# Kernel tuning notes

Hardware: AMD Instinct MI355X
Metric: run time of the kernel (lower is better)

Reference implementation:

```python
import jax, jax.numpy as jnp
import numpy as np

B, H, S, D = 4, 16, 2048, 128
NEG = -1000000000.0


def setup_inputs() -> dict:
    key = jax.random.key(0)
    kq, kk, kv, km = jax.random.split(key, 4)
    Q = jax.random.normal(kq, (B, H, S, D), dtype=jnp.float32)
    K = jax.random.normal(kk, (B, H, S, D), dtype=jnp.float32)
    V = jax.random.normal(kv, (B, H, S, D), dtype=jnp.float32)
    mask = jax.random.randint(km, (B, 1, S, S), 0, 2, dtype=jnp.int32)
    return {"Q": Q, "K": K, "V": V, "mask": mask}


def reference(Q, K, V, mask):
    # NOTE: original module computes d_k but never scales -> no 1/sqrt(d_k).
    scores = jnp.einsum("bhqd,bhkd->bhqk", Q, K)  # [B,H,S,S]
    scores = jnp.where(mask == 0, NEG, scores)
    attn = jax.nn.softmax(scores, axis=-1)
    out = jnp.einsum("bhqk,bhkd->bhqd", attn, V)  # [B,H,S,D]
    return out
```

## Files before the change

kernel.cpp:

```cpp
#include <hip/hip_runtime.h>
#include <hip/hip_bf16.h>

#define B_ 4
#define H_ 16
#define S_ 2048
#define D_ 128
#define NEGV -1000000000.0f
#define LOG2E 1.44269504f
#define THR 9.0f

typedef _Float16 f16;
typedef __attribute__((ext_vector_type(8))) _Float16 f16x8;
typedef __attribute__((ext_vector_type(4))) _Float16 f16x4v;
typedef __attribute__((ext_vector_type(2))) __fp16 fp16x2_b;
typedef __attribute__((ext_vector_type(4))) float f32x4;

__device__ inline unsigned int pack2h(float lo, float hi){
  union { f16 h[2]; unsigned int u; } cv;
  cv.h[0] = (f16)lo; cv.h[1] = (f16)hi;
  return cv.u;
}
__device__ inline unsigned short f2h16(float x){
  union { f16 h; unsigned short u; } cv; cv.h = (f16)x; return cv.u;
}
__device__ inline unsigned int pkrtz(float a, float b){
  union { fp16x2_b h; unsigned int u; } cv;
  cv.h = __builtin_amdgcn_cvt_pkrtz(a, b);
  return cv.u;
}
__device__ inline void async16(void* l, const void* g){
  __builtin_amdgcn_global_load_lds(
      (const __attribute__((address_space(1))) unsigned int*)g,
      (__attribute__((address_space(3))) unsigned int*)l, 16, 0, 0);
}

constexpr size_t MBW     = (size_t)B_*S_*(S_/32);
constexpr size_t KBYTES  = (size_t)B_*H_*S_*D_*2;
constexpr size_t WS_MID  = MBW*4 + 2*KBYTES;

__global__ __launch_bounds__(256)
void prepass(const float* __restrict__ K, const float* __restrict__ V,
             const int* __restrict__ mask, unsigned int* __restrict__ mbits,
             char* __restrict__ wsK, char* __restrict__ wsV)
{
  __shared__ char Vim[16384];
  int bid = blockIdx.x, tid = threadIdx.x;
  size_t base = (size_t)bid * (64*128);
  const float* kp = K + base;
  char* ok = wsK + (size_t)bid*16384;
  #pragma unroll
  for (int j = 0; j < 8; ++j){
    int f = tid + j*256; int kr = f>>5, c = f&31;
    float4 v = *(const float4*)(kp + kr*128 + c*4);
    unsigned int lo = pack2h(v.x, v.y), hi = pack2h(v.z, v.w);
    int off = (kr*256 + c*8) ^ ((kr&7)<<4);
    *(uint2*)(ok + off) = make_uint2(lo, hi);
  }
  const float* vp = V + base;
  #pragma unroll
  for (int j = 0; j < 8; ++j){
    int f = tid + j*256; int k = f>>5, c = f&31;
    float4 v = *(const float4*)(vp + k*128 + c*4);
    float e[4] = {v.x, v.y, v.z, v.w};
    #pragma unroll
    for (int u = 0; u < 4; ++u){
      int d = c*4 + u;
      *(unsigned short*)(Vim + d*128 + ((2*k) ^ ((d&7)<<4))) = f2h16(e[u]);
    }
  }
  __syncthreads();
  char* ov = wsV + (size_t)bid*16384;
  #pragma unroll
  for (int j = 0; j < 4; ++j)
    *(uint4*)(ov + tid*16 + j*4096) = *(const uint4*)(Vim + tid*16 + j*4096);
  {
    size_t wdx = (size_t)bid*256 + tid;
    const int* p = mask + wdx*32;
    unsigned int o = 0;
    #pragma unroll
    for (int i = 0; i < 32; i += 4){
      int4 m4 = *(const int4*)(p + i);
      o |= (m4.x ? 1u<<i : 0u) | (m4.y ? 1u<<(i+1) : 0u)
         | (m4.z ? 1u<<(i+2) : 0u) | (m4.w ? 1u<<(i+3) : 0u);
    }
    mbits[wdx] = o;
  }
}

__global__ __launch_bounds__(256, 2)
void attn_fast(const float* __restrict__ Q,
               const unsigned long long* __restrict__ mbits,
               const char* __restrict__ wsK, const char* __restrict__ wsV,
               float* __restrict__ out)
{
  __shared__ char KB[2][16384];
  __shared__ char VB[2][16384];
  __shared__ char PL[8192];

  int bid = blockIdx.x;
  int wg = (bid & 7) * 128 + (bid >> 3);
  int bh = wg >> 4, qb = wg & 15;
  int b  = bh >> 4;
  int tid = threadIdx.x;
  int w = tid >> 6, lane = tid & 63;
  int g = lane >> 4, r = lane & 15;
  int sw = (r & 7) << 4;
  size_t base = (size_t)bh * (S_*D_);
  int qg0 = qb*128 + w*32 + r;
  int qg1 = qg0 + 16;

  f16x8 qf[2][4];
  #pragma unroll
  for (int u = 0; u < 2; ++u){
    const float* qp = Q + base + (size_t)(u ? qg1 : qg0) * D_;
    #pragma unroll
    for (int dc = 0; dc < 4; ++dc){
      float4 a = *(const float4*)(qp + dc*32 + g*8);
      float4 c = *(const float4*)(qp + dc*32 + g*8 + 4);
      f16x8 q8;
      q8[0]=(f16)a.x; q8[1]=(f16)a.y; q8[2]=(f16)a.z; q8[3]=(f16)a.w;
      q8[4]=(f16)c.x; q8[5]=(f16)c.y; q8[6]=(f16)c.z; q8[7]=(f16)c.w;
      qf[u][dc] = q8;
    }
  }

  const char* gK = wsK + (size_t)(bh*32)*16384 + tid*16;
  const char* gV = wsV + (size_t)(bh*32)*16384 + tid*16;
  const unsigned long long* mr0 = mbits + ((size_t)b*S_ + qg0)*32;
  const unsigned long long* mr1 = mbits + ((size_t)b*S_ + qg1)*32;

  f32x4 stc[2][4];
  unsigned long long mwc0 = mr0[0], mwc1 = mr1[0];
  #pragma unroll
  for (int u = 0; u < 2; ++u)
    #pragma unroll
    for (int t = 0; t < 4; ++t) stc[u][t] = (f32x4){0.f,0.f,0.f,0.f};
  #pragma unroll
  for (int j = 0; j < 4; ++j){
    async16(&KB[0][tid*16 + j*4096], gK + j*4096);
    async16(&VB[0][tid*16 + j*4096], gV + j*4096);
  }

  float m0 = -3.0e38f, m1 = -3.0e38f;
  f32x4 acc[2][8];
  f32x4 accl[2];
  #pragma unroll
  for (int u = 0; u < 2; ++u){
    accl[u] = (f32x4){0.f,0.f,0.f,0.f};
    #pragma unroll
    for (int i = 0; i < 8; ++i) acc[u][i] = (f32x4){0.f,0.f,0.f,0.f};
  }
  f16x8 ones;
  #pragma unroll
  for (int i = 0; i < 8; ++i) ones[i] = (f16)1.0f;

  unsigned long long mwn0 = 0, mwn1 = 0;

  for (int kb = 0; kb < 32; ++kb){
    int cur = kb & 1;
    if (kb < 31){
      mwn0 = mr0[kb+1]; mwn1 = mr1[kb+1];
      const char* gk = gK + (size_t)(kb+1)*16384;
      const char* gv = gV + (size_t)(kb+1)*16384;
      #pragma unroll
      for (int j = 0; j < 4; ++j){
        async16(&KB[cur^1][tid*16 + j*4096], gk + j*4096);
        async16(&VB[cur^1][tid*16 + j*4096], gv + j*4096);
      }
      asm volatile("s_waitcnt vmcnt(10)" ::: "memory");
    } else {
      asm volatile("s_waitcnt vmcnt(0)" ::: "memory");
    }
    __builtin_amdgcn_s_barrier();

    const char* kbuf = KB[cur];
    const char* vbuf = VB[cur];

    __builtin_amdgcn_s_setprio(1);
    #pragma unroll
    for (int t = 0; t < 4; ++t){
      int rb = (t*16 + r)*256;
      #pragma unroll
      for (int dc = 0; dc < 4; ++dc){
        f16x8 kf = *(const f16x8*)(kbuf + rb + ((dc*64 + g*16) ^ sw));
        stc[0][t] = __builtin_amdgcn_mfma_f32_16x16x32_f16(kf, qf[0][dc], stc[0][t], 0, 0, 0);
        stc[1][t] = __builtin_amdgcn_mfma_f32_16x16x32_f16(kf, qf[1][dc], stc[1][t], 0, 0, 0);
      }
    }
    __builtin_amdgcn_s_setprio(0);

    #pragma unroll
    for (int u = 0; u < 2; ++u){
      unsigned long long mw = u ? mwc1 : mwc0;
      unsigned int mlo = (unsigned int)(mw >> (g*4));
      unsigned int mhi = (unsigned int)(mw >> (g*4 + 32));
      #pragma unroll
      for (int t = 0; t < 4; ++t){
        unsigned int tv = (t & 2) ? mhi : mlo;
        int sh = (t & 1) * 16;
        #pragma unroll
        for (int i = 0; i < 4; ++i)
          if (!((tv >> (sh + i)) & 1u)) stc[u][t][i] = NEGV;
      }
    }

    float pmax0 = stc[0][0][0], pmax1 = stc[1][0][0];
    #pragma unroll
    for (int t = 0; t < 4; ++t)
      #pragma unroll
      for (int i = 0; i < 4; ++i){
        pmax0 = fmaxf(pmax0, stc[0][t][i]);
        pmax1 = fmaxf(pmax1, stc[1][t][i]);
      }
    pmax0 = fmaxf(pmax0, __shfl_xor(pmax0, 16));
    pmax0 = fmaxf(pmax0, __shfl_xor(pmax0, 32));
    pmax1 = fmaxf(pmax1, __shfl_xor(pmax1, 16));
    pmax1 = fmaxf(pmax1, __shfl_xor(pmax1, 32));

    bool need = (pmax0 > m0 + THR) || (pmax1 > m1 + THR);
    if (__ballot(need)){
      float n0 = fmaxf(m0, pmax0), n1 = fmaxf(m1, pmax1);
      float cr0 = __builtin_amdgcn_exp2f((m0 - n0) * LOG2E);
      float cr1 = __builtin_amdgcn_exp2f((m1 - n1) * LOG2E);
      float cj0[4], cj1[4];
      #pragma unroll
      for (int j = 0; j < 4; ++j){
        cj0[j] = __shfl(cr0, g*4 + j);
        cj1[j] = __shfl(cr1, g*4 + j);
      }
      #pragma unroll
      for (int dt = 0; dt < 8; ++dt)
        #pragma unroll
        for (int j = 0; j < 4; ++j){
          acc[0][dt][j] *= cj0[j];
          acc[1][dt][j] *= cj1[j];
        }
      #pragma unroll
      for (int j = 0; j < 4; ++j){
        accl[0][j] *= cj0[j];
        accl[1][j] *= cj1[j];
      }
      m0 = n0; m1 = n1;
    }
    float mL0 = m0 * LOG2E, mL1 = m1 * LOG2E;

    char* prow = PL + (w*16 + r)*128;
    f16x8 pf[2][2];
    #pragma unroll
    for (int u = 0; u < 2; ++u){
      float mL = u ? mL1 : mL0;
      #pragma unroll
      for (int t = 0; t < 4; ++t){
        float p0 = __builtin_amdgcn_exp2f(__builtin_fmaf(stc[u][t][0], LOG2E, -mL));
        float p1 = __builtin_amdgcn_exp2f(__builtin_fmaf(stc[u][t][1], LOG2E, -mL));
        float p2 = __builtin_amdgcn_exp2f(__builtin_fmaf(stc[u][t][2], LOG2E, -mL));
        float p3 = __builtin_amdgcn_exp2f(__builtin_fmaf(stc[u][t][3], LOG2E, -mL));
        *(uint2*)(prow + ((t*32 + g*8) ^ sw)) = make_uint2(pkrtz(p0,p1), pkrtz(p2,p3));
      }
      pf[u][0] = *(const f16x8*)(prow + ((g*16) ^ sw));
      pf[u][1] = *(const f16x8*)(prow + ((64 + g*16) ^ sw));
    }

    accl[0] = __builtin_amdgcn_mfma_f32_16x16x32_f16(pf[0][0], ones, accl[0], 0, 0, 0);
    accl[0] = __builtin_amdgcn_mfma_f32_16x16x32_f16(pf[0][1], ones, accl[0], 0, 0, 0);
    accl[1] = __builtin_amdgcn_mfma_f32_16x16x32_f16(pf[1][0], ones, accl[1], 0, 0, 0);
    accl[1] = __builtin_amdgcn_mfma_f32_16x16x32_f16(pf[1][1], ones, accl[1], 0, 0, 0);

    __builtin_amdgcn_s_setprio(1);
    #pragma unroll
    for (int dt = 0; dt < 8; ++dt){
      int vr = (dt*16 + r)*128;
      f16x8 v0 = *(const f16x8*)(vbuf + vr + ((g*16) ^ sw));
      f16x8 v1 = *(const f16x8*)(vbuf + vr + ((64 + g*16) ^ sw));
      acc[0][dt] = __builtin_amdgcn_mfma_f32_16x16x32_f16(pf[0][0], v0, acc[0][dt], 0, 0, 0);
      acc[0][dt] = __builtin_amdgcn_mfma_f32_16x16x32_f16(pf[0][1], v1, acc[0][dt], 0, 0, 0);
      acc[1][dt] = __builtin_amdgcn_mfma_f32_16x16x32_f16(pf[1][0], v0, acc[1][dt], 0, 0, 0);
      acc[1][dt] = __builtin_amdgcn_mfma_f32_16x16x32_f16(pf[1][1], v1, acc[1][dt], 0, 0, 0);
    }
    __builtin_amdgcn_s_setprio(0);

    mwc0 = mwn0; mwc1 = mwn1;
    #pragma unroll
    for (int u = 0; u < 2; ++u)
      #pragma unroll
      for (int t = 0; t < 4; ++t) stc[u][t] = (f32x4){0.f,0.f,0.f,0.f};
    __builtin_amdgcn_s_barrier();
  }

  #pragma unroll
  for (int u = 0; u < 2; ++u){
    float inv[4];
    #pragma unroll
    for (int j = 0; j < 4; ++j) inv[j] = 1.f / accl[u][j];
    size_t ob = base + (size_t)(qb*128 + w*32 + u*16) * D_;
    #pragma unroll
    for (int dt = 0; dt < 8; ++dt){
      int d = dt*16 + r;
      #pragma unroll
      for (int j = 0; j < 4; ++j)
        out[ob + (size_t)(g*4 + j)*D_ + d] = acc[u][dt][j] * inv[j];
    }
  }
}

constexpr int VTS = 68;
constexpr int PSS = 72;

__global__ __launch_bounds__(256)
void attn_fwd(const float* __restrict__ Q, const float* __restrict__ K,
              const float* __restrict__ V, const int* __restrict__ mask,
              float* __restrict__ out)
{
  __shared__ unsigned short Klds[64 * D_];
  __shared__ unsigned short Vt[D_ * VTS];
  __shared__ unsigned short Plds[4 * 16 * PSS];

  int bid = blockIdx.x;
  int wg = (bid & 7) * 256 + (bid >> 3);
  int bh = wg >> 5, qb = wg & 31;
  int b  = bh >> 4;
  int tid = threadIdx.x;
  int w = tid >> 6, lane = tid & 63;
  int g = lane >> 4, r = lane & 15;
  size_t base = (size_t)bh * S_ * D_;
  int qg = qb * 64 + w * 16 + r;

  f16x8 qf[4];
  {
    const float* qp = Q + base + (size_t)qg * D_;
    #pragma unroll
    for (int dc = 0; dc < 4; ++dc){
      float4 a = *reinterpret_cast<const float4*>(qp + dc*32 + g*8);
      float4 c = *reinterpret_cast<const float4*>(qp + dc*32 + g*8 + 4);
      f16x8 q8;
      q8[0]=(f16)a.x; q8[1]=(f16)a.y; q8[2]=(f16)a.z; q8[3]=(f16)a.w;
      q8[4]=(f16)c.x; q8[5]=(f16)c.y; q8[6]=(f16)c.z; q8[7]=(f16)c.w;
      qf[dc] = q8;
    }
  }

  float mrun = -3.0e38f, lrun = 0.f;
  f32x4 acc[8];
  #pragma unroll
  for (int i = 0; i < 8; ++i) acc[i] = (f32x4){0.f,0.f,0.f,0.f};

  for (int kb = 0; kb < S_/64; ++kb){
    const float* kp = K + base + (size_t)(kb*64) * D_;
    #pragma unroll
    for (int i = 0; i < 8; ++i){
      int f = tid + i*256;
      int kr = f >> 5, c = f & 31;
      float4 v = *reinterpret_cast<const float4*>(kp + kr*D_ + c*4);
      unsigned int lo = pack2h(v.x, v.y), hi = pack2h(v.z, v.w);
      int off = (kr*256 + c*8) ^ ((kr & 7) << 4);
      *reinterpret_cast<uint2*>(reinterpret_cast<char*>(Klds) + off) = make_uint2(lo, hi);
    }
    const float* vp = V + base + (size_t)(kb*64) * D_;
    #pragma unroll
    for (int i = 0; i < 4; ++i){
      int f = tid + i*256;
      int p = f >> 5, c = f & 31;
      float4 v0 = *reinterpret_cast<const float4*>(vp + (size_t)(2*p)*D_ + c*4);
      float4 v1 = *reinterpret_cast<const float4*>(vp + (size_t)(2*p+1)*D_ + c*4);
      float e0[4] = {v0.x, v0.y, v0.z, v0.w};
      float e1[4] = {v1.x, v1.y, v1.z, v1.w};
      #pragma unroll
      for (int j = 0; j < 4; ++j){
        int d = c*4 + j;
        *reinterpret_cast<unsigned int*>(reinterpret_cast<char*>(Vt) + (d*VTS + 2*p)*2)
            = pack2h(e0[j], e1[j]);
      }
    }
    __syncthreads();

    f32x4 st[4];
    #pragma unroll
    for (int t = 0; t < 4; ++t){
      f32x4 s = (f32x4){0.f,0.f,0.f,0.f};
      int row = t*16 + r;
      #pragma unroll
      for (int dc = 0; dc < 4; ++dc){
        int off = row*256 + ((dc*64 + g*16) ^ ((row & 7) << 4));
        f16x8 kf = *reinterpret_cast<const f16x8*>(reinterpret_cast<const char*>(Klds) + off);
        s = __builtin_amdgcn_mfma_f32_16x16x32_f16(kf, qf[dc], s, 0, 0, 0);
      }
      st[t] = s;
    }

    #pragma unroll
    for (int t = 0; t < 4; ++t){
      int4 m4 = *reinterpret_cast<const int4*>(
          mask + ((size_t)b * S_ + qg) * S_ + kb*64 + t*16 + g*4);
      if (!m4.x) st[t][0] = NEGV;
      if (!m4.y) st[t][1] = NEGV;
      if (!m4.z) st[t][2] = NEGV;
      if (!m4.w) st[t][3] = NEGV;
    }

    float pmax = st[0][0];
    #pragma unroll
    for (int t = 0; t < 4; ++t)
      #pragma unroll
      for (int i = 0; i < 4; ++i) pmax = fmaxf(pmax, st[t][i]);
    pmax = fmaxf(pmax, __shfl_xor(pmax, 16));
    pmax = fmaxf(pmax, __shfl_xor(pmax, 32));
    float mnew = fmaxf(mrun, pmax);
    float corr = __builtin_amdgcn_exp2f((mrun - mnew) * LOG2E);
    float psum = 0.f;
    char* prow = reinterpret_cast<char*>(Plds) + (size_t)(w*16 + r)*PSS*2;
    #pragma unroll
    for (int t = 0; t < 4; ++t){
      float p0 = __builtin_amdgcn_exp2f((st[t][0]-mnew)*LOG2E);
      float p1 = __builtin_amdgcn_exp2f((st[t][1]-mnew)*LOG2E);
      float p2 = __builtin_amdgcn_exp2f((st[t][2]-mnew)*LOG2E);
      float p3 = __builtin_amdgcn_exp2f((st[t][3]-mnew)*LOG2E);
      psum += (p0+p1)+(p2+p3);
      char* pb = prow + (t*16 + g*4)*2;
      *reinterpret_cast<unsigned int*>(pb)     = pack2h(p0, p1);
      *reinterpret_cast<unsigned int*>(pb + 4) = pack2h(p2, p3);
    }
    psum += __shfl_xor(psum, 16);
    psum += __shfl_xor(psum, 32);
    lrun = lrun * corr + psum;
    mrun = mnew;
    float cq0 = __shfl(corr, g*4 + 0);
    float cq1 = __shfl(corr, g*4 + 1);
    float cq2 = __shfl(corr, g*4 + 2);
    float cq3 = __shfl(corr, g*4 + 3);
    #pragma unroll
    for (int dt = 0; dt < 8; ++dt){
      acc[dt][0] *= cq0; acc[dt][1] *= cq1; acc[dt][2] *= cq2; acc[dt][3] *= cq3;
    }

    f16x8 pf0 = *reinterpret_cast<const f16x8*>(prow + g*16);
    f16x8 pf1 = *reinterpret_cast<const f16x8*>(prow + 64 + g*16);
    #pragma unroll
    for (int dt = 0; dt < 8; ++dt){
      int vo = (dt*16 + r)*VTS*2 + g*16;
      const char* vb = reinterpret_cast<const char*>(Vt);
      union { f16x8 v; f16x4v h[2]; } uv0, uv1;
      uv0.h[0] = *reinterpret_cast<const f16x4v*>(vb + vo);
      uv0.h[1] = *reinterpret_cast<const f16x4v*>(vb + vo + 8);
      acc[dt] = __builtin_amdgcn_mfma_f32_16x16x32_f16(pf0, uv0.v, acc[dt], 0, 0, 0);
      uv1.h[0] = *reinterpret_cast<const f16x4v*>(vb + vo + 64);
      uv1.h[1] = *reinterpret_cast<const f16x4v*>(vb + vo + 72);
      acc[dt] = __builtin_amdgcn_mfma_f32_16x16x32_f16(pf1, uv1.v, acc[dt], 0, 0, 0);
    }
    __syncthreads();
  }

  float l0 = __shfl(lrun, g*4 + 0);
  float l1 = __shfl(lrun, g*4 + 1);
  float l2 = __shfl(lrun, g*4 + 2);
  float l3 = __shfl(lrun, g*4 + 3);
  float i0 = 1.f/l0, i1 = 1.f/l1, i2 = 1.f/l2, i3 = 1.f/l3;
  size_t obase = base + (size_t)(qb*64 + w*16) * D_;
  #pragma unroll
  for (int dt = 0; dt < 8; ++dt){
    int d = dt*16 + r;
    out[obase + (size_t)(g*4 + 0)*D_ + d] = acc[dt][0]*i0;
    out[obase + (size_t)(g*4 + 1)*D_ + d] = acc[dt][1]*i1;
    out[obase + (size_t)(g*4 + 2)*D_ + d] = acc[dt][2]*i2;
    out[obase + (size_t)(g*4 + 3)*D_ + d] = acc[dt][3]*i3;
  }
}

extern "C" void kernel_launch(void* const* d_in, const int* in_sizes, int n_in,
                              void* d_out, int out_size, void* d_ws, size_t ws_size,
                              hipStream_t stream) {
  const float* Q = (const float*)d_in[0];
  const float* K = (const float*)d_in[1];
  const float* V = (const float*)d_in[2];
  const int* mask = (const int*)d_in[3];
  float* out = (float*)d_out;
  dim3 blk(256);

  if (ws_size >= WS_MID){
    unsigned int* mbits = (unsigned int*)d_ws;
    char* wsK = (char*)d_ws + MBW*4;
    char* wsV = wsK + KBYTES;
    prepass<<<dim3(2048), blk, 0, stream>>>(K, V, mask, mbits, wsK, wsV);
    attn_fast<<<dim3(1024), blk, 0, stream>>>(Q, (const unsigned long long*)d_ws,
                                              wsK, wsV, out);
  } else {
    attn_fwd<<<dim3(2048), blk, 0, stream>>>(Q, K, V, mask, out);
  }
}
```

Measured before the change: 249.3 us.

## Halve key block to 32 to shrink LDS and registers for higher occupancy

Reduces the KV tile per iteration from 64 to 32 keys in both the prepass layout and the main attention loop. LDS use drops to about half and per-thread score registers shrink, so launch bounds are raised to allow 4 workgroups per CU. Swizzle offsets are precomputed outside the loop and mask words become 32-bit. In exchange the loop runs twice as many iterations, with twice as many barriers, global prefetches and online-softmax max and rescale steps.

```diff
diff --git a/kernel.cpp b/kernel.cpp
--- a/kernel.cpp
+++ b/kernel.cpp
@@ -43,38 +43,38 @@
              const int* __restrict__ mask, unsigned int* __restrict__ mbits,
              char* __restrict__ wsK, char* __restrict__ wsV)
 {
-  __shared__ char Vim[16384];
+  __shared__ char Vim[8192];
   int bid = blockIdx.x, tid = threadIdx.x;
-  size_t base = (size_t)bid * (64*128);
+  size_t base = (size_t)bid * (32*128);
   const float* kp = K + base;
-  char* ok = wsK + (size_t)bid*16384;
-  #pragma unroll
-  for (int j = 0; j < 8; ++j){
+  char* ok = wsK + (size_t)bid*8192;
+  #pragma unroll
+  for (int j = 0; j < 4; ++j){
     int f = tid + j*256; int kr = f>>5, c = f&31;
     float4 v = *(const float4*)(kp + kr*128 + c*4);
     unsigned int lo = pack2h(v.x, v.y), hi = pack2h(v.z, v.w);
-    int off = (kr*256 + c*8) ^ ((kr&7)<<4);
+    int off = kr*256 + ((c*8) ^ ((kr&7)<<4));
     *(uint2*)(ok + off) = make_uint2(lo, hi);
   }
   const float* vp = V + base;
   #pragma unroll
-  for (int j = 0; j < 8; ++j){
+  for (int j = 0; j < 4; ++j){
     int f = tid + j*256; int k = f>>5, c = f&31;
     float4 v = *(const float4*)(vp + k*128 + c*4);
     float e[4] = {v.x, v.y, v.z, v.w};
     #pragma unroll
     for (int u = 0; u < 4; ++u){
       int d = c*4 + u;
-      *(unsigned short*)(Vim + d*128 + ((2*k) ^ ((d&7)<<4))) = f2h16(e[u]);
+      *(unsigned short*)(Vim + d*64 + ((2*k) ^ ((d&3)<<4))) = f2h16(e[u]);
     }
   }
   __syncthreads();
-  char* ov = wsV + (size_t)bid*16384;
-  #pragma unroll
-  for (int j = 0; j < 4; ++j)
+  char* ov = wsV + (size_t)bid*8192;
+  #pragma unroll
+  for (int j = 0; j < 2; ++j)
     *(uint4*)(ov + tid*16 + j*4096) = *(const uint4*)(Vim + tid*16 + j*4096);
-  {
-    size_t wdx = (size_t)bid*256 + tid;
+  if (tid < 128){
+    size_t wdx = (size_t)bid*128 + tid;
     const int* p = mask + wdx*32;
     unsigned int o = 0;
     #pragma unroll
@@ -87,15 +87,15 @@
   }
 }
 
-__global__ __launch_bounds__(256, 2)
+__global__ __launch_bounds__(256, 4)
 void attn_fast(const float* __restrict__ Q,
-               const unsigned long long* __restrict__ mbits,
+               const unsigned int* __restrict__ mbits,
                const char* __restrict__ wsK, const char* __restrict__ wsV,
                float* __restrict__ out)
 {
-  __shared__ char KB[2][16384];
-  __shared__ char VB[2][16384];
-  __shared__ char PL[8192];
+  __shared__ char KB[2][8192];
+  __shared__ char VB[2][8192];
+  __shared__ char PL[4096];
 
   int bid = blockIdx.x;
   int wg = (bid & 7) * 128 + (bid >> 3);
@@ -104,10 +104,21 @@
   int tid = threadIdx.x;
   int w = tid >> 6, lane = tid & 63;
   int g = lane >> 4, r = lane & 15;
-  int sw = (r & 7) << 4;
+  int swk = (r & 7) << 4;
+  int swp = (r & 3) << 4;
+  int sh4 = g * 4;
   size_t base = (size_t)bh * (S_*D_);
   int qg0 = qb*128 + w*32 + r;
   int qg1 = qg0 + 16;
+  char* prow = PL + (w*16 + r)*64;
+
+  int xq0 = (g*16) ^ swk;
+  int xq1 = (64 + g*16) ^ swk;
+  int xq2 = (128 + g*16) ^ swk;
+  int xq3 = (192 + g*16) ^ swk;
+  int xpt0 = (g*8) ^ swp;
+  int xpt1 = (32 + g*8) ^ swp;
+  int xqp = (g*16) ^ swp;
 
   f16x8 qf[2][4];
   #pragma unroll
@@ -124,19 +135,14 @@
     }
   }
 
-  const char* gK = wsK + (size_t)(bh*32)*16384 + tid*16;
-  const char* gV = wsV + (size_t)(bh*32)*16384 + tid*16;
-  const unsigned long long* mr0 = mbits + ((size_t)b*S_ + qg0)*32;
-  const unsigned long long* mr1 = mbits + ((size_t)b*S_ + qg1)*32;
-
-  f32x4 stc[2][4];
-  unsigned long long mwc0 = mr0[0], mwc1 = mr1[0];
-  #pragma unroll
-  for (int u = 0; u < 2; ++u)
-    #pragma unroll
-    for (int t = 0; t < 4; ++t) stc[u][t] = (f32x4){0.f,0.f,0.f,0.f};
-  #pragma unroll
-  for (int j = 0; j < 4; ++j){
+  const char* gK = wsK + (size_t)(bh*64)*8192 + tid*16;
+  const char* gV = wsV + (size_t)(bh*64)*8192 + tid*16;
+  const unsigned int* mr0 = mbits + ((size_t)b*S_ + qg0)*64;
+  const unsigned int* mr1 = mbits + ((size_t)b*S_ + qg1)*64;
+
+  unsigned int mwc0 = mr0[0], mwc1 = mr1[0];
+  #pragma unroll
+  for (int j = 0; j < 2; ++j){
     async16(&KB[0][tid*16 + j*4096], gK + j*4096);
     async16(&VB[0][tid*16 + j*4096], gV + j*4096);
   }
@@ -144,30 +150,31 @@
   float m0 = -3.0e38f, m1 = -3.0e38f;
   f32x4 acc[2][8];
   f32x4 accl[2];
+  f32x4 z4 = (f32x4){0.f,0.f,0.f,0.f};
   #pragma unroll
   for (int u = 0; u < 2; ++u){
-    accl[u] = (f32x4){0.f,0.f,0.f,0.f};
-    #pragma unroll
-    for (int i = 0; i < 8; ++i) acc[u][i] = (f32x4){0.f,0.f,0.f,0.f};
+    accl[u] = z4;
+    #pragma unroll
+    for (int i = 0; i < 8; ++i) acc[u][i] = z4;
   }
   f16x8 ones;
   #pragma unroll
   for (int i = 0; i < 8; ++i) ones[i] = (f16)1.0f;
 
-  unsigned long long mwn0 = 0, mwn1 = 0;
-
-  for (int kb = 0; kb < 32; ++kb){
+  unsigned int mwn0 = 0, mwn1 = 0;
+
+  for (int kb = 0; kb < 64; ++kb){
     int cur = kb & 1;
-    if (kb < 31){
+    if (kb < 63){
       mwn0 = mr0[kb+1]; mwn1 = mr1[kb+1];
-      const char* gk = gK + (size_t)(kb+1)*16384;
-      const char* gv = gV + (size_t)(kb+1)*16384;
-      #pragma unroll
-      for (int j = 0; j < 4; ++j){
+      const char* gk = gK + (size_t)(kb+1)*8192;
+      const char* gv = gV + (size_t)(kb+1)*8192;
+      #pragma unroll
+      for (int j = 0; j < 2; ++j){
         async16(&KB[cur^1][tid*16 + j*4096], gk + j*4096);
         async16(&VB[cur^1][tid*16 + j*4096], gv + j*4096);
       }
-      asm volatile("s_waitcnt vmcnt(10)" ::: "memory");
+      asm volatile("s_waitcnt vmcnt(6)" ::: "memory");
     } else {
       asm volatile("s_waitcnt vmcnt(0)" ::: "memory");
     }
@@ -176,42 +183,42 @@
     const char* kbuf = KB[cur];
     const char* vbuf = VB[cur];
 
+    f32x4 st[2][2];
     __builtin_amdgcn_s_setprio(1);
     #pragma unroll
-    for (int t = 0; t < 4; ++t){
-      int rb = (t*16 + r)*256;
-      #pragma unroll
-      for (int dc = 0; dc < 4; ++dc){
-        f16x8 kf = *(const f16x8*)(kbuf + rb + ((dc*64 + g*16) ^ sw));
-        stc[0][t] = __builtin_amdgcn_mfma_f32_16x16x32_f16(kf, qf[0][dc], stc[0][t], 0, 0, 0);
-        stc[1][t] = __builtin_amdgcn_mfma_f32_16x16x32_f16(kf, qf[1][dc], stc[1][t], 0, 0, 0);
-      }
+    for (int t = 0; t < 2; ++t){
+      const char* kr_ = kbuf + (t*16 + r)*256;
+      f16x8 kf = *(const f16x8*)(kr_ + xq0);
+      st[0][t] = __builtin_amdgcn_mfma_f32_16x16x32_f16(kf, qf[0][0], z4, 0, 0, 0);
+      st[1][t] = __builtin_amdgcn_mfma_f32_16x16x32_f16(kf, qf[1][0], z4, 0, 0, 0);
+      kf = *(const f16x8*)(kr_ + xq1);
+      st[0][t] = __builtin_amdgcn_mfma_f32_16x16x32_f16(kf, qf[0][1], st[0][t], 0, 0, 0);
+      st[1][t] = __builtin_amdgcn_mfma_f32_16x16x32_f16(kf, qf[1][1], st[1][t], 0, 0, 0);
+      kf = *(const f16x8*)(kr_ + xq2);
+      st[0][t] = __builtin_amdgcn_mfma_f32_16x16x32_f16(kf, qf[0][2], st[0][t], 0, 0, 0);
+      st[1][t] = __builtin_amdgcn_mfma_f32_16x16x32_f16(kf, qf[1][2], st[1][t], 0, 0, 0);
+      kf = *(const f16x8*)(kr_ + xq3);
+      st[0][t] = __builtin_amdgcn_mfma_f32_16x16x32_f16(kf, qf[0][3], st[0][t], 0, 0, 0);
+      st[1][t] = __builtin_amdgcn_mfma_f32_16x16x32_f16(kf, qf[1][3], st[1][t], 0, 0, 0);
     }
     __builtin_amdgcn_s_setprio(0);
 
     #pragma unroll
     for (int u = 0; u < 2; ++u){
-      unsigned long long mw = u ? mwc1 : mwc0;
-      unsigned int mlo = (unsigned int)(mw >> (g*4));
-      unsigned int mhi = (unsigned int)(mw >> (g*4 + 32));
-      #pragma unroll
-      for (int t = 0; t < 4; ++t){
-        unsigned int tv = (t & 2) ? mhi : mlo;
-        int sh = (t & 1) * 16;
-        #pragma unroll
-        for (int i = 0; i < 4; ++i)
-          if (!((tv >> (sh + i)) & 1u)) stc[u][t][i] = NEGV;
-      }
-    }
-
-    float pmax0 = stc[0][0][0], pmax1 = stc[1][0][0];
-    #pragma unroll
-    for (int t = 0; t < 4; ++t)
+      unsigned int mw = u ? mwc1 : mwc0;
+      unsigned int tv0 = mw >> sh4;
+      unsigned int tv1 = mw >> (16 + sh4);
       #pragma unroll
       for (int i = 0; i < 4; ++i){
-        pmax0 = fmaxf(pmax0, stc[0][t][i]);
-        pmax1 = fmaxf(pmax1, stc[1][t][i]);
-      }
+        if (!((tv0 >> i) & 1u)) st[u][0][i] = NEGV;
+        if (!((tv1 >> i) & 1u)) st[u][1][i] = NEGV;
+      }
+    }
+
+    float pmax0 = fmaxf(fmaxf(fmaxf(st[0][0][0], st[0][0][1]), fmaxf(st[0][0][2], st[0][0][3])),
+                        fmaxf(fmaxf(st[0][1][0], st[0][1][1]), fmaxf(st[0][1][2], st[0][1][3])));
+    float pmax1 = fmaxf(fmaxf(fmaxf(st[1][0][0], st[1][0][1]), fmaxf(st[1][0][2], st[1][0][3])),
+                        fmaxf(fmaxf(st[1][1][0], st[1][1][1]), fmaxf(st[1][1][2], st[1][1][3])));
     pmax0 = fmaxf(pmax0, __shfl_xor(pmax0, 16));
     pmax0 = fmaxf(pmax0, __shfl_xor(pmax0, 32));
     pmax1 = fmaxf(pmax1, __shfl_xor(pmax1, 16));
@@ -225,8 +232,8 @@
       float cj0[4], cj1[4];
       #pragma unroll
       for (int j = 0; j < 4; ++j){
-        cj0[j] = __shfl(cr0, g*4 + j);
-        cj1[j] = __shfl(cr1, g*4 + j);
+        cj0[j] = __shfl(cr0, sh4 + j);
+        cj1[j] = __shfl(cr1, sh4 + j);
       }
       #pragma unroll
       for (int dt = 0; dt < 8; ++dt)
@@ -244,46 +251,38 @@
     }
     float mL0 = m0 * LOG2E, mL1 = m1 * LOG2E;
 
-    char* prow = PL + (w*16 + r)*128;
-    f16x8 pf[2][2];
+    f16x8 pf[2];
     #pragma unroll
     for (int u = 0; u < 2; ++u){
       float mL = u ? mL1 : mL0;
-      #pragma unroll
-      for (int t = 0; t < 4; ++t){
-        float p0 = __builtin_amdgcn_exp2f(__builtin_fmaf(stc[u][t][0], LOG2E, -mL));
-        float p1 = __builtin_amdgcn_exp2f(__builtin_fmaf(stc[u][t][1], LOG2E, -mL));
-        float p2 = __builtin_amdgcn_exp2f(__builtin_fmaf(stc[u][t][2], LOG2E, -mL));
-        float p3 = __builtin_amdgcn_exp2f(__builtin_fmaf(stc[u][t][3], LOG2E, -mL));
-        *(uint2*)(prow + ((t*32 + g*8) ^ sw)) = make_uint2(pkrtz(p0,p1), pkrtz(p2,p3));
-      }
-      pf[u][0] = *(const f16x8*)(prow + ((g*16) ^ sw));
-      pf[u][1] = *(const f16x8*)(prow + ((64 + g*16) ^ sw));
-    }
-
-    accl[0] = __builtin_amdgcn_mfma_f32_16x16x32_f16(pf[0][0], ones, accl[0], 0, 0, 0);
-    accl[0] = __builtin_amdgcn_mfma_f32_16x16x32_f16(pf[0][1], ones, accl[0], 0, 0, 0);
-    accl[1] = __builtin_amdgcn_mfma_f32_16x16x32_f16(pf[1][0], ones, accl[1], 0, 0, 0);
-    accl[1] = __builtin_amdgcn_mfma_f32_16x16x32_f16(pf[1][1], ones, accl[1], 0, 0, 0);
+      {
+        float p0 = __builtin_amdgcn_exp2f(__builtin_fmaf(st[u][0][0], LOG2E, -mL));
+        float p1 = __builtin_amdgcn_exp2f(__builtin_fmaf(st[u][0][1], LOG2E, -mL));
+        float p2 = __builtin_amdgcn_exp2f(__builtin_fmaf(st[u][0][2], LOG2E, -mL));
+        float p3 = __builtin_amdgcn_exp2f(__builtin_fmaf(st[u][0][3], LOG2E, -mL));
+        *(uint2*)(prow + xpt0) = make_uint2(pkrtz(p0,p1), pkrtz(p2,p3));
+        p0 = __builtin_amdgcn_exp2f(__builtin_fmaf(st[u][1][0], LOG2E, -mL));
+        p1 = __builtin_amdgcn_exp2f(__builtin_fmaf(st[u][1][1], LOG2E, -mL));
+        p2 = __builtin_amdgcn_exp2f(__builtin_fmaf(st[u][1][2], LOG2E, -mL));
+        p3 = __builtin_amdgcn_exp2f(__builtin_fmaf(st[u][1][3], LOG2E, -mL));
+        *(uint2*)(prow + xpt1) = make_uint2(pkrtz(p0,p1), pkrtz(p2,p3));
+      }
+      pf[u] = *(const f16x8*)(prow + xqp);
+    }
+
+    accl[0] = __builtin_amdgcn_mfma_f32_16x16x32_f16(pf[0], ones, accl[0], 0, 0, 0);
+    accl[1] = __builtin_amdgcn_mfma_f32_16x16x32_f16(pf[1], ones, accl[1], 0, 0, 0);
 
     __builtin_amdgcn_s_setprio(1);
     #pragma unroll
     for (int dt = 0; dt < 8; ++dt){
-      int vr = (dt*16 + r)*128;
-      f16x8 v0 = *(const f16x8*)(vbuf + vr + ((g*16) ^ sw));
-      f16x8 v1 = *(const f16x8*)(vbuf + vr + ((64 + g*16) ^ sw));
-      acc[0][dt] = __builtin_amdgcn_mfma_f32_16x16x32_f16(pf[0][0], v0, acc[0][dt], 0, 0, 0);
-      acc[0][dt] = __builtin_amdgcn_mfma_f32_16x16x32_f16(pf[0][1], v1, acc[0][dt], 0, 0, 0);
-      acc[1][dt] = __builtin_amdgcn_mfma_f32_16x16x32_f16(pf[1][0], v0, acc[1][dt], 0, 0, 0);
-      acc[1][dt] = __builtin_amdgcn_mfma_f32_16x16x32_f16(pf[1][1], v1, acc[1][dt], 0, 0, 0);
+      f16x8 v0 = *(const f16x8*)(vbuf + (dt*16 + r)*64 + xqp);
+      acc[0][dt] = __builtin_amdgcn_mfma_f32_16x16x32_f16(pf[0], v0, acc[0][dt], 0, 0, 0);
+      acc[1][dt] = __builtin_amdgcn_mfma_f32_16x16x32_f16(pf[1], v0, acc[1][dt], 0, 0, 0);
     }
     __builtin_amdgcn_s_setprio(0);
 
     mwc0 = mwn0; mwc1 = mwn1;
-    #pragma unroll
-    for (int u = 0; u < 2; ++u)
-      #pragma unroll
-      for (int t = 0; t < 4; ++t) stc[u][t] = (f32x4){0.f,0.f,0.f,0.f};
     __builtin_amdgcn_s_barrier();
   }
 
@@ -298,7 +297,7 @@
       int d = dt*16 + r;
       #pragma unroll
       for (int j = 0; j < 4; ++j)
-        out[ob + (size_t)(g*4 + j)*D_ + d] = acc[u][dt][j] * inv[j];
+        out[ob + (size_t)(sh4 + j)*D_ + d] = acc[u][dt][j] * inv[j];
     }
   }
 }
@@ -473,16 +472,14 @@
   const float* V = (const float*)d_in[2];
   const int* mask = (const int*)d_in[3];
   float* out = (float*)d_out;
-  dim3 blk(256);
 
   if (ws_size >= WS_MID){
     unsigned int* mbits = (unsigned int*)d_ws;
     char* wsK = (char*)d_ws + MBW*4;
     char* wsV = wsK + KBYTES;
-    prepass<<<dim3(2048), blk, 0, stream>>>(K, V, mask, mbits, wsK, wsV);
-    attn_fast<<<dim3(1024), blk, 0, stream>>>(Q, (const unsigned long long*)d_ws,
-                                              wsK, wsV, out);
+    prepass<<<dim3(4096), dim3(256), 0, stream>>>(K, V, mask, mbits, wsK, wsV);
+    attn_fast<<<dim3(1024), dim3(256), 0, stream>>>(Q, mbits, wsK, wsV, out);
   } else {
-    attn_fwd<<<dim3(2048), blk, 0, stream>>>(Q, K, V, mask, out);
-  }
-}
+    attn_fwd<<<dim3(2048), dim3(256), 0, stream>>>(Q, K, V, mask, out);
+  }
+}
```

New measurement: 747.2 us. +199.7%, slower.
